# Kernel optimization log

Hardware: AMD Instinct MI355X
Metric: run time of the kernel (lower is better)

The kernel has to match this reference:

```python
import jax, jax.numpy as jnp
import numpy as np

B, S, H, C, T = 8, 1024, 256, 4, 12
THETA = 10000.0


def setup_inputs() -> dict:
    key = jax.random.key(0)
    ks = jax.random.split(key, 7)
    x = jax.random.normal(ks[0], (B, S, H), dtype=jnp.float32)
    token_index = jax.random.randint(ks[1], (B, S), 0, 256, dtype=jnp.int32)
    thread_id = jnp.sort(jax.random.randint(ks[2], (B, S), 0, T, dtype=jnp.int32), axis=-1)
    bound = 1.0 / np.sqrt(H)  # nn.Linear default init range
    Wq = jax.random.uniform(ks[3], (H, H * C), jnp.float32, -bound, bound)
    bq = jax.random.uniform(ks[4], (H * C,), jnp.float32, -bound, bound)
    Wk = jax.random.uniform(ks[5], (H, H * C), jnp.float32, -bound, bound)
    bk = jax.random.uniform(ks[6], (H * C,), jnp.float32, -bound, bound)
    return {"x": x, "Wq": Wq, "bq": bq, "Wk": Wk, "bk": bk,
            "token_index": token_index, "thread_id": thread_id}


def _rope(v, pos):
    # v: (B, S, C, H); pos: (B, S) signed positions
    half = v.shape[-1] // 2
    # freqs = 1 / theta^(arange(0, H, 2) / H)
    freqs = 1.0 / (THETA ** (jnp.arange(half, dtype=jnp.float32) * 2.0 / (2 * half)))
    ang = pos[..., None].astype(jnp.float32) * freqs          # (B, S, half)
    cos = jnp.cos(ang)[:, :, None, :]                          # (B, S, 1, half)
    sin = jnp.sin(ang)[:, :, None, :]
    vr = v.reshape(*v.shape[:-1], half, 2)                     # complex pairs (even, odd)
    re = vr[..., 0] * cos - vr[..., 1] * sin
    im = vr[..., 0] * sin + vr[..., 1] * cos
    return jnp.stack([re, im], axis=-1).reshape(v.shape)


def reference(x, Wq, bq, Wk, bk, token_index, thread_id):
    q = (x @ Wq + bq).reshape(B, S, C, H)
    k = (x @ Wk + bk).reshape(B, S, C, H)
    # Block sign rules of get_instance_embedding reduce to three cases per
    # token pair (m, n) with thread ids ti=thread(m), tj=thread(n):
    #   0 < ti < tj : q uses -pos, k uses +pos
    #   0 < tj < ti : q uses +pos, k uses -pos
    #   otherwise   : both use +pos
    q_pos = _rope(q, token_index)
    q_neg = _rope(q, -token_index)
    k_pos = _rope(k, token_index)
    k_neg = _rope(k, -token_index)
    l1 = jnp.einsum('bmch,bnch->bcmn', q_pos, k_pos)
    l2 = jnp.einsum('bmch,bnch->bcmn', q_neg, k_pos)
    l3 = jnp.einsum('bmch,bnch->bcmn', q_pos, k_neg)
    ti = thread_id[:, :, None]   # rows
    tj = thread_id[:, None, :]   # cols
    cond2 = ((ti > 0) & (ti < tj))[:, None, :, :]   # (B,1,S,S)
    cond3 = ((tj > 0) & (ti > tj))[:, None, :, :]
    return jnp.where(cond2, l2, jnp.where(cond3, l3, l1))  # (B, C, S, S)
```

## Files before the change

### kernel.cpp

```cpp
#include <hip/hip_runtime.h>

#define BB 8
#define SS 1024
#define HH 256
#define CC 4
#define NQ 1024

typedef unsigned short u16;
typedef unsigned int u32;
typedef __attribute__((ext_vector_type(8))) __bf16 bf16x8;
typedef __attribute__((ext_vector_type(4))) float f32x4;
typedef __attribute__((ext_vector_type(4))) u32 u32x4;
typedef __attribute__((ext_vector_type(4))) u16 u16x4;

__device__ __forceinline__ u16 f2bf(float f) {
    u32 u = __float_as_uint(f);
    u32 r = (u + 0x7FFFu + ((u >> 16) & 1u)) >> 16;
    return (u16)r;
}

__device__ __forceinline__ void gld16(const u16* g, u16* l) {
    __builtin_amdgcn_global_load_lds(
        (const __attribute__((address_space(1))) void*)g,
        (__attribute__((address_space(3))) void*)l, 16, 0, 0);
}

__device__ __forceinline__ bf16x8 ldsfrag32(const u16* smem, int row, int c16) {
    const char* p = (const char*)smem + row * 64 + (((c16 ^ ((row >> 1) & 3)) & 3) << 4);
    return *(const bf16x8*)p;
}

#define WAITV(n) asm volatile("s_waitcnt vmcnt(" #n ")" ::: "memory")
#define WAITLG() asm volatile("s_waitcnt lgkmcnt(0)" ::: "memory")

__global__ void __launch_bounds__(256) k0_prep(
    const float4* __restrict__ x4, u16x4* __restrict__ xbf4,
    const float* __restrict__ Wq, const float* __restrict__ Wk,
    u16* __restrict__ Wt, float2* __restrict__ trig) {
    __shared__ u16 tl[64][65];
    int b = blockIdx.x;
    if (b < 2048) {
        int i = b * 256 + threadIdx.x;
        float4 v = x4[i];
        u16x4 o = {f2bf(v.x), f2bf(v.y), f2bf(v.z), f2bf(v.w)};
        xbf4[i] = o;
    } else if (b < 2176) {
        int idx = b - 2048;
        int nb = (idx & 31) * 64, kb = (idx >> 5) * 64;
        int c = threadIdx.x & 63;
#pragma unroll
        for (int r = threadIdx.x >> 6; r < 64; r += 4) {
            int k = kb + r, n = nb + c;
            float v = (n < NQ) ? Wq[k * NQ + n] : Wk[k * NQ + (n - NQ)];
            tl[c][r] = f2bf(v);
        }
        __syncthreads();
#pragma unroll
        for (int r = threadIdx.x >> 6; r < 64; r += 4) {
            Wt[(size_t)(nb + r) * HH + kb + c] = tl[r][c];
        }
    } else {
        int i = (b - 2176) * 256 + threadIdx.x;
        int pos = i >> 7, f = i & 127;
        float freq = __expf(-(float)f * 0.07195578515529633f);
        float ang = (float)pos * freq;
        float s, c;
        sincosf(ang, &s, &c);
        trig[i] = make_float2(c, s);
    }
}

#define STAGE32(dst, srcbase, roff, kc) do {                                    \
        int r_ = (threadIdx.x >> 2);                                            \
        int sl_ = (threadIdx.x & 3) ^ ((r_ >> 1) & 3);                          \
        gld16((srcbase) + (size_t)((roff) + r_) * HH + (kc) * 32 + sl_ * 8,     \
              (dst) + ww * 512);                                                \
    } while (0)

__global__ void __launch_bounds__(512, 2) k1_proj(
    const u16* __restrict__ xbf, const u16* __restrict__ Wt,
    const float* __restrict__ bq, const float* __restrict__ bk,
    const int* __restrict__ tok, const float2* __restrict__ trig,
    u16* __restrict__ qpos, u16* __restrict__ qneg,
    u16* __restrict__ kpos, u16* __restrict__ kneg) {
    int h = blockIdx.x;
    int logical = (h & 7) * 128 + (h >> 3);
    int m0 = (logical >> 4) * 128, n0 = (logical & 15) * 128;
    int ww = threadIdx.x >> 6, l = threadIdx.x & 63;
    int wr = ww >> 1, wc = ww & 1;

    __shared__ u16 sm[24576];
    u16* bA[3] = {sm, sm + 8192, sm + 16384};

    f32x4 acc[2][4] = {};
    STAGE32(bA[0], xbf, m0, 0); STAGE32(bA[0] + 4096, Wt, n0, 0);
    STAGE32(bA[1], xbf, m0, 1); STAGE32(bA[1] + 4096, Wt, n0, 1);
    STAGE32(bA[2], xbf, m0, 2); STAGE32(bA[2] + 4096, Wt, n0, 2);
    WAITV(4);
    __builtin_amdgcn_s_barrier();
#pragma unroll
    for (int kc = 0; kc < 8; ++kc) {
        const u16* As = bA[kc % 3];
        const u16* Bs = As + 4096;
        int c16 = l >> 4;
        bf16x8 af[2], bfr[4];
        __builtin_amdgcn_s_setprio(1);
#pragma unroll
        for (int mi = 0; mi < 2; ++mi) af[mi] = ldsfrag32(As, wr * 32 + mi * 16 + (l & 15), c16);
#pragma unroll
        for (int ns = 0; ns < 4; ++ns) bfr[ns] = ldsfrag32(Bs, wc * 64 + ns * 16 + (l & 15), c16);
#pragma unroll
        for (int mi = 0; mi < 2; ++mi)
#pragma unroll
            for (int ns = 0; ns < 4; ++ns)
                acc[mi][ns] = __builtin_amdgcn_mfma_f32_16x16x32_bf16(af[mi], bfr[ns], acc[mi][ns], 0, 0, 0);
        __builtin_amdgcn_s_setprio(0);
        if (kc < 7) {
            WAITLG();
            __builtin_amdgcn_s_barrier();
            if (kc < 5) {
                STAGE32(bA[kc % 3], xbf, m0, kc + 3);
                STAGE32(bA[kc % 3] + 4096, Wt, n0, kc + 3);
                WAITV(4);
            } else if (kc == 5) {
                WAITV(2);
            } else {
                WAITV(0);
            }
            __builtin_amdgcn_s_barrier();
        }
    }

#pragma unroll
    for (int mi = 0; mi < 2; ++mi)
#pragma unroll
        for (int ns = 0; ns < 4; ++ns) {
            int n = n0 + wc * 64 + ns * 16 + (l & 15);
            bool isq = n < NQ;
            int nc = n & (NQ - 1);
            float bias = isq ? bq[nc] : bk[nc];
            int c = nc >> 8, hh = nc & 255, fi = hh >> 1;
#pragma unroll
            for (int r = 0; r < 4; ++r) {
                int m = m0 + wr * 32 + mi * 16 + (l >> 4) * 4 + r;
                float val = acc[mi][ns][r] + bias;
                float other = __shfl_xor(val, 1);
                int pos = tok[m];
                float2 cs = trig[pos * 128 + fi];
                float rp, rn;
                if ((l & 1) == 0) {
                    rp = val * cs.x - other * cs.y;
                    rn = val * cs.x + other * cs.y;
                } else {
                    rp = other * cs.y + val * cs.x;
                    rn = -other * cs.y + val * cs.x;
                }
                int b = m >> 10, s = m & 1023;
                size_t oidx = ((size_t)((b << 2) | c) * SS + s) * HH + hh;
                if (isq) {
                    qpos[oidx] = f2bf(rp);
                    qneg[oidx] = f2bf(rn);
                } else {
                    kpos[oidx] = f2bf(rp);
                    kneg[oidx] = f2bf(rn);
                }
            }
        }
}

__global__ void __launch_bounds__(512, 2) k2_gemm(
    const u16* __restrict__ qpos, const u16* __restrict__ qneg,
    const u16* __restrict__ kpos, const u16* __restrict__ kneg,
    const int* __restrict__ thread_id, float* __restrict__ out) {
    int h = blockIdx.x;
    int logical = (h & 7) * 256 + (h >> 3);
    int bc = logical >> 6;
    int t = logical & 63;
    int m0 = (t >> 3) * 128, n0 = (t & 7) * 128;
    const int* tb = thread_id + (bc >> 2) * SS;
    int ww = threadIdx.x >> 6, l = threadIdx.x & 63;
    int wr = ww >> 1, wc = ww & 1;
    int ti0 = tb[m0], ti1 = tb[m0 + 127], tj0 = tb[n0], tj1 = tb[n0 + 127];
    bool pure2 = (ti0 > 0) & (ti1 < tj0);
    bool pure3 = (tj0 > 0) & (ti0 > tj1);
    bool pure1 = (ti1 == 0) | (tj1 == 0) | ((ti0 == ti1) & (tj0 == tj1) & (ti0 == tj0));
    size_t base = (size_t)bc * (SS * HH);
    float* ob = out + (size_t)bc * ((size_t)SS * SS);
    int ar0 = m0 + wr * 32;
    int nb0 = n0 + wc * 64;

    __shared__ u16 sm[32768];

    if (pure1 | pure2 | pure3) {
        const u16* q = (pure2 ? qneg : qpos) + base;
        const u16* k = (pure3 ? kneg : kpos) + base;
        u16* bA[3] = {sm, sm + 8192, sm + 16384};

        f32x4 acc[2][4] = {};
        STAGE32(bA[0], q, m0, 0); STAGE32(bA[0] + 4096, k, n0, 0);
        STAGE32(bA[1], q, m0, 1); STAGE32(bA[1] + 4096, k, n0, 1);
        STAGE32(bA[2], q, m0, 2); STAGE32(bA[2] + 4096, k, n0, 2);
        WAITV(4);
        __builtin_amdgcn_s_barrier();
#pragma unroll
        for (int kc = 0; kc < 8; ++kc) {
            const u16* As = bA[kc % 3];
            const u16* Bs = As + 4096;
            int c16 = l >> 4;
            bf16x8 af[2], bfr[4];
            __builtin_amdgcn_s_setprio(1);
#pragma unroll
            for (int mi = 0; mi < 2; ++mi) af[mi] = ldsfrag32(As, wr * 32 + mi * 16 + (l & 15), c16);
#pragma unroll
            for (int ns = 0; ns < 4; ++ns) bfr[ns] = ldsfrag32(Bs, wc * 64 + ns * 16 + (l & 15), c16);
#pragma unroll
            for (int mi = 0; mi < 2; ++mi)
#pragma unroll
                for (int ns = 0; ns < 4; ++ns)
                    acc[mi][ns] = __builtin_amdgcn_mfma_f32_16x16x32_bf16(af[mi], bfr[ns], acc[mi][ns], 0, 0, 0);
            __builtin_amdgcn_s_setprio(0);
            if (kc < 7) {
                WAITLG();
                __builtin_amdgcn_s_barrier();
                if (kc < 5) {
                    STAGE32(bA[kc % 3], q, m0, kc + 3);
                    STAGE32(bA[kc % 3] + 4096, k, n0, kc + 3);
                    WAITV(4);
                } else if (kc == 5) {
                    WAITV(2);
                } else {
                    WAITV(0);
                }
                __builtin_amdgcn_s_barrier();
            }
        }

#pragma unroll
        for (int mi = 0; mi < 2; ++mi)
#pragma unroll
            for (int ns = 0; ns < 4; ++ns)
#pragma unroll
                for (int r = 0; r < 4; ++r) {
                    int m = ar0 + mi * 16 + (l >> 4) * 4 + r;
                    int n = nb0 + ns * 16 + (l & 15);
                    __builtin_nontemporal_store(acc[mi][ns][r], &ob[(size_t)m * SS + n]);
                }
    } else {
        const u16* qp = qpos + base;
        const u16* qn = qneg + base;
        const u16* kp = kpos + base;
        const u16* kn = kneg + base;
        u16* bufb[2] = {sm, sm + 16384};

        int bamin = ti0 > 1 ? ti0 : 1;
        int bcmin = tj0 > 1 ? tj0 : 1;
        bool B2 = (ti1 > 0) && (tj1 > bamin);
        bool B3 = (tj1 > 0) && (ti1 > bcmin);

        int fa[2], fb[2], fc[4], fd[4];
#pragma unroll
        for (int mi = 0; mi < 2; ++mi) {
            fa[mi] = tb[ar0 + mi * 16];
            fb[mi] = tb[ar0 + mi * 16 + 15];
        }
#pragma unroll
        for (int ns = 0; ns < 4; ++ns) {
            fc[ns] = tb[nb0 + ns * 16];
            fd[ns] = tb[nb0 + ns * 16 + 15];
        }
        u32 msk1 = 0, msk2 = 0, msk3 = 0;
#pragma unroll
        for (int mi = 0; mi < 2; ++mi)
#pragma unroll
            for (int ns = 0; ns < 4; ++ns) {
                u32 bit = 1u << (mi * 4 + ns);
                if ((fa[mi] == 0) | (fc[ns] == 0) | ((fa[mi] <= fd[ns]) & (fc[ns] <= fb[mi]))) msk1 |= bit;
                int amin = fa[mi] > 1 ? fa[mi] : 1;
                if ((fb[mi] > 0) & (fd[ns] > amin)) msk2 |= bit;
                int cmin = fc[ns] > 1 ? fc[ns] : 1;
                if ((fd[ns] > 0) & (fb[mi] > cmin)) msk3 |= bit;
            }
        msk1 = __builtin_amdgcn_readfirstlane(msk1);
        msk2 = __builtin_amdgcn_readfirstlane(msk2);
        msk3 = __builtin_amdgcn_readfirstlane(msk3);

#define MSTAGE(bi, kc) do {                                \
        STAGE32(bufb[bi], qp, m0, kc);                     \
        if (B2) STAGE32(bufb[bi] + 4096, qn, m0, kc);      \
        STAGE32(bufb[bi] + 8192, kp, n0, kc);              \
        if (B3) STAGE32(bufb[bi] + 12288, kn, n0, kc);     \
    } while (0)
#define WAITN() do {                                       \
        if (B2 & B3) { WAITV(4); }                         \
        else if (B2 | B3) { WAITV(3); }                    \
        else { WAITV(2); }                                 \
    } while (0)

        f32x4 a1[2][4] = {}, a2[2][4] = {}, a3[2][4] = {};
        MSTAGE(0, 0);
        MSTAGE(1, 1);
        WAITN();
        __builtin_amdgcn_s_barrier();
#pragma unroll
        for (int kc = 0; kc < 8; ++kc) {
            const u16* bqp = bufb[kc & 1];
            const u16* bqn = bqp + 4096;
            const u16* bkp = bqp + 8192;
            const u16* bkn = bqp + 12288;
            int c16 = l >> 4;
            bf16x8 qpF[2], qnF[2], kpF[4], knF[4];
            __builtin_amdgcn_s_setprio(1);
#pragma unroll
            for (int mi = 0; mi < 2; ++mi) {
                int rr = wr * 32 + mi * 16 + (l & 15);
                qpF[mi] = ldsfrag32(bqp, rr, c16);
                if (msk2) qnF[mi] = ldsfrag32(bqn, rr, c16);
            }
#pragma unroll
            for (int ns = 0; ns < 4; ++ns) {
                int rn = wc * 64 + ns * 16 + (l & 15);
                kpF[ns] = ldsfrag32(bkp, rn, c16);
                if (msk3) knF[ns] = ldsfrag32(bkn, rn, c16);
            }
#pragma unroll
            for (int mi = 0; mi < 2; ++mi)
#pragma unroll
                for (int ns = 0; ns < 4; ++ns) {
                    u32 bit = 1u << (mi * 4 + ns);
                    if (msk1 & bit)
                        a1[mi][ns] = __builtin_amdgcn_mfma_f32_16x16x32_bf16(qpF[mi], kpF[ns], a1[mi][ns], 0, 0, 0);
                    if (msk2 & bit)
                        a2[mi][ns] = __builtin_amdgcn_mfma_f32_16x16x32_bf16(qnF[mi], kpF[ns], a2[mi][ns], 0, 0, 0);
                    if (msk3 & bit)
                        a3[mi][ns] = __builtin_amdgcn_mfma_f32_16x16x32_bf16(qpF[mi], knF[ns], a3[mi][ns], 0, 0, 0);
                }
            __builtin_amdgcn_s_setprio(0);
            if (kc < 7) {
                WAITLG();
                __builtin_amdgcn_s_barrier();
                if (kc < 6) {
                    MSTAGE(kc & 1, kc + 2);
                    WAITN();
                } else {
                    WAITV(0);
                }
                __builtin_amdgcn_s_barrier();
            }
        }
#undef MSTAGE
#undef WAITN

        int tj[4], ti_[2][4];
#pragma unroll
        for (int ns = 0; ns < 4; ++ns) tj[ns] = tb[nb0 + ns * 16 + (l & 15)];
#pragma unroll
        for (int mi = 0; mi < 2; ++mi)
#pragma unroll
            for (int r = 0; r < 4; ++r) ti_[mi][r] = tb[ar0 + mi * 16 + (l >> 4) * 4 + r];

#pragma unroll
        for (int mi = 0; mi < 2; ++mi)
#pragma unroll
            for (int ns = 0; ns < 4; ++ns)
#pragma unroll
                for (int r = 0; r < 4; ++r) {
                    int m = ar0 + mi * 16 + (l >> 4) * 4 + r;
                    int n = nb0 + ns * 16 + (l & 15);
                    int ti = ti_[mi][r], tjj = tj[ns];
                    float v = (ti > 0 && ti < tjj) ? a2[mi][ns][r]
                             : ((tjj > 0 && ti > tjj) ? a3[mi][ns][r] : a1[mi][ns][r]);
                    __builtin_nontemporal_store(v, &ob[(size_t)m * SS + n]);
                }
    }
}

extern "C" void kernel_launch(void* const* d_in, const int* in_sizes, int n_in,
                              void* d_out, int out_size, void* d_ws, size_t ws_size,
                              hipStream_t stream) {
    const float* x  = (const float*)d_in[0];
    const float* Wq = (const float*)d_in[1];
    const float* bq = (const float*)d_in[2];
    const float* Wk = (const float*)d_in[3];
    const float* bk = (const float*)d_in[4];
    const int* tok  = (const int*)d_in[5];
    const int* tid  = (const int*)d_in[6];
    float* out = (float*)d_out;

    char* ws = (char*)d_ws;
    const size_t MB = 1u << 20;
    u16* qpos = (u16*)(ws);
    u16* qneg = (u16*)(ws + 16 * MB);
    u16* kpos = (u16*)(ws + 32 * MB);
    u16* kneg = (u16*)(ws + 48 * MB);
    u16* xbf  = (u16*)(ws + 64 * MB);
    u16* Wt   = (u16*)(ws + 68 * MB);
    float2* trig = (float2*)(ws + 69 * MB);

    k0_prep<<<2304, 256, 0, stream>>>((const float4*)x, (u16x4*)xbf, Wq, Wk, Wt, trig);
    k1_proj<<<1024, 512, 0, stream>>>(xbf, Wt, bq, bk, tok, trig, qpos, qneg, kpos, kneg);
    k2_gemm<<<2048, 512, 0, stream>>>(qpos, qneg, kpos, kneg, tid, out);
}
```

Baseline: 111.4 us.

## Split pure/mixed tile paths into separate kernels with 256-thread 4x4-fragment waves

The projection GEMM and the pure-case attention GEMM move to 256-thread blocks where each wave computes a 64x64 tile (4x4 MFMA fragments) instead of 32x64. They also switch from triple to double buffering, which halves LDS use. The pure and mixed tile cases, which used to share one kernel, are now two kernels. The mixed kernel keeps its 512-thread layout and large LDS footprint, so it no longer limits occupancy for the pure tiles. The cost is an extra kernel launch in which blocks exit early, plus higher register pressure per wave.

```diff
diff --git a/kernel.cpp b/kernel.cpp
--- a/kernel.cpp
+++ b/kernel.cpp
@@ -70,6 +70,14 @@
     }
 }
 
+#define KST(dst, srcbase, roff, kc)                                             \
+    _Pragma("unroll") for (int i_ = 0; i_ < 2; ++i_) {                          \
+        int sid_ = i_ * 256 + (int)threadIdx.x;                                 \
+        int r_ = sid_ >> 2;                                                     \
+        int sl_ = (sid_ & 3) ^ ((r_ >> 1) & 3);                                 \
+        gld16((srcbase) + (size_t)((roff) + r_) * HH + (kc) * 32 + sl_ * 8,     \
+              (dst) + i_ * 2048 + ww * 512);                                    \
+    }
 #define STAGE32(dst, srcbase, roff, kc) do {                                    \
         int r_ = (threadIdx.x >> 2);                                            \
         int sl_ = (threadIdx.x & 3) ^ ((r_ >> 1) & 3);                          \
@@ -77,7 +85,7 @@
               (dst) + ww * 512);                                                \
     } while (0)
 
-__global__ void __launch_bounds__(512, 2) k1_proj(
+__global__ void __launch_bounds__(256, 4) k1_proj(
     const u16* __restrict__ xbf, const u16* __restrict__ Wt,
     const float* __restrict__ bq, const float* __restrict__ bk,
     const int* __restrict__ tok, const float2* __restrict__ trig,
@@ -89,28 +97,26 @@
     int ww = threadIdx.x >> 6, l = threadIdx.x & 63;
     int wr = ww >> 1, wc = ww & 1;
 
-    __shared__ u16 sm[24576];
-    u16* bA[3] = {sm, sm + 8192, sm + 16384};
-
-    f32x4 acc[2][4] = {};
-    STAGE32(bA[0], xbf, m0, 0); STAGE32(bA[0] + 4096, Wt, n0, 0);
-    STAGE32(bA[1], xbf, m0, 1); STAGE32(bA[1] + 4096, Wt, n0, 1);
-    STAGE32(bA[2], xbf, m0, 2); STAGE32(bA[2] + 4096, Wt, n0, 2);
+    __shared__ u16 sm[16384];
+
+    f32x4 acc[4][4] = {};
+    KST(sm, xbf, m0, 0)          KST(sm + 4096, Wt, n0, 0)
+    KST(sm + 8192, xbf, m0, 1)   KST(sm + 12288, Wt, n0, 1)
     WAITV(4);
     __builtin_amdgcn_s_barrier();
 #pragma unroll
     for (int kc = 0; kc < 8; ++kc) {
-        const u16* As = bA[kc % 3];
+        const u16* As = sm + (kc & 1) * 8192;
         const u16* Bs = As + 4096;
         int c16 = l >> 4;
-        bf16x8 af[2], bfr[4];
+        bf16x8 af[4], bfr[4];
         __builtin_amdgcn_s_setprio(1);
 #pragma unroll
-        for (int mi = 0; mi < 2; ++mi) af[mi] = ldsfrag32(As, wr * 32 + mi * 16 + (l & 15), c16);
+        for (int mi = 0; mi < 4; ++mi) af[mi] = ldsfrag32(As, wr * 64 + mi * 16 + (l & 15), c16);
 #pragma unroll
         for (int ns = 0; ns < 4; ++ns) bfr[ns] = ldsfrag32(Bs, wc * 64 + ns * 16 + (l & 15), c16);
 #pragma unroll
-        for (int mi = 0; mi < 2; ++mi)
+        for (int mi = 0; mi < 4; ++mi)
 #pragma unroll
             for (int ns = 0; ns < 4; ++ns)
                 acc[mi][ns] = __builtin_amdgcn_mfma_f32_16x16x32_bf16(af[mi], bfr[ns], acc[mi][ns], 0, 0, 0);
@@ -118,12 +124,11 @@
         if (kc < 7) {
             WAITLG();
             __builtin_amdgcn_s_barrier();
-            if (kc < 5) {
-                STAGE32(bA[kc % 3], xbf, m0, kc + 3);
-                STAGE32(bA[kc % 3] + 4096, Wt, n0, kc + 3);
+            if (kc < 6) {
+                u16* db = sm + (kc & 1) * 8192;
+                KST(db, xbf, m0, kc + 2)
+                KST(db + 4096, Wt, n0, kc + 2)
                 WAITV(4);
-            } else if (kc == 5) {
-                WAITV(2);
             } else {
                 WAITV(0);
             }
@@ -132,7 +137,7 @@
     }
 
 #pragma unroll
-    for (int mi = 0; mi < 2; ++mi)
+    for (int mi = 0; mi < 4; ++mi)
 #pragma unroll
         for (int ns = 0; ns < 4; ++ns) {
             int n = n0 + wc * 64 + ns * 16 + (l & 15);
@@ -142,7 +147,7 @@
             int c = nc >> 8, hh = nc & 255, fi = hh >> 1;
 #pragma unroll
             for (int r = 0; r < 4; ++r) {
-                int m = m0 + wr * 32 + mi * 16 + (l >> 4) * 4 + r;
+                int m = m0 + wr * 64 + mi * 16 + (l >> 4) * 4 + r;
                 float val = acc[mi][ns][r] + bias;
                 float other = __shfl_xor(val, 1);
                 int pos = tok[m];
@@ -168,7 +173,7 @@
         }
 }
 
-__global__ void __launch_bounds__(512, 2) k2_gemm(
+__global__ void __launch_bounds__(256, 4) k2_pure(
     const u16* __restrict__ qpos, const u16* __restrict__ qneg,
     const u16* __restrict__ kpos, const u16* __restrict__ kneg,
     const int* __restrict__ thread_id, float* __restrict__ out) {
@@ -178,111 +183,135 @@
     int t = logical & 63;
     int m0 = (t >> 3) * 128, n0 = (t & 7) * 128;
     const int* tb = thread_id + (bc >> 2) * SS;
-    int ww = threadIdx.x >> 6, l = threadIdx.x & 63;
-    int wr = ww >> 1, wc = ww & 1;
     int ti0 = tb[m0], ti1 = tb[m0 + 127], tj0 = tb[n0], tj1 = tb[n0 + 127];
     bool pure2 = (ti0 > 0) & (ti1 < tj0);
     bool pure3 = (tj0 > 0) & (ti0 > tj1);
     bool pure1 = (ti1 == 0) | (tj1 == 0) | ((ti0 == ti1) & (tj0 == tj1) & (ti0 == tj0));
+    if (!(pure1 | pure2 | pure3)) return;
+
+    size_t base = (size_t)bc * (SS * HH);
+    const u16* q = (pure2 ? qneg : qpos) + base;
+    const u16* k = (pure3 ? kneg : kpos) + base;
+    float* ob = out + (size_t)bc * ((size_t)SS * SS);
+
+    int ww = threadIdx.x >> 6, l = threadIdx.x & 63;
+    int wr = ww >> 1, wc = ww & 1;
+    int ar0 = m0 + wr * 64;
+    int nb0 = n0 + wc * 64;
+
+    __shared__ u16 sm[16384];
+
+    f32x4 acc[4][4] = {};
+    KST(sm, q, m0, 0)          KST(sm + 4096, k, n0, 0)
+    KST(sm + 8192, q, m0, 1)   KST(sm + 12288, k, n0, 1)
+    WAITV(4);
+    __builtin_amdgcn_s_barrier();
+#pragma unroll
+    for (int kc = 0; kc < 8; ++kc) {
+        const u16* As = sm + (kc & 1) * 8192;
+        const u16* Bs = As + 4096;
+        int c16 = l >> 4;
+        bf16x8 af[4], bfr[4];
+        __builtin_amdgcn_s_setprio(1);
+#pragma unroll
+        for (int mi = 0; mi < 4; ++mi) af[mi] = ldsfrag32(As, wr * 64 + mi * 16 + (l & 15), c16);
+#pragma unroll
+        for (int ns = 0; ns < 4; ++ns) bfr[ns] = ldsfrag32(Bs, wc * 64 + ns * 16 + (l & 15), c16);
+#pragma unroll
+        for (int mi = 0; mi < 4; ++mi)
+#pragma unroll
+            for (int ns = 0; ns < 4; ++ns)
+                acc[mi][ns] = __builtin_amdgcn_mfma_f32_16x16x32_bf16(af[mi], bfr[ns], acc[mi][ns], 0, 0, 0);
+        __builtin_amdgcn_s_setprio(0);
+        if (kc < 7) {
+            WAITLG();
+            __builtin_amdgcn_s_barrier();
+            if (kc < 6) {
+                u16* db = sm + (kc & 1) * 8192;
+                KST(db, q, m0, kc + 2)
+                KST(db + 4096, k, n0, kc + 2)
+                WAITV(4);
+            } else {
+                WAITV(0);
+            }
+            __builtin_amdgcn_s_barrier();
+        }
+    }
+
+#pragma unroll
+    for (int mi = 0; mi < 4; ++mi)
+#pragma unroll
+        for (int ns = 0; ns < 4; ++ns)
+#pragma unroll
+            for (int r = 0; r < 4; ++r) {
+                int m = ar0 + mi * 16 + (l >> 4) * 4 + r;
+                int n = nb0 + ns * 16 + (l & 15);
+                __builtin_nontemporal_store(acc[mi][ns][r], &ob[(size_t)m * SS + n]);
+            }
+}
+
+__global__ void __launch_bounds__(512, 2) k2_mixed(
+    const u16* __restrict__ qpos, const u16* __restrict__ qneg,
+    const u16* __restrict__ kpos, const u16* __restrict__ kneg,
+    const int* __restrict__ thread_id, float* __restrict__ out) {
+    int h = blockIdx.x;
+    int logical = (h & 7) * 256 + (h >> 3);
+    int bc = logical >> 6;
+    int t = logical & 63;
+    int m0 = (t >> 3) * 128, n0 = (t & 7) * 128;
+    const int* tb = thread_id + (bc >> 2) * SS;
+    int ti0 = tb[m0], ti1 = tb[m0 + 127], tj0 = tb[n0], tj1 = tb[n0 + 127];
+    bool pure2 = (ti0 > 0) & (ti1 < tj0);
+    bool pure3 = (tj0 > 0) & (ti0 > tj1);
+    bool pure1 = (ti1 == 0) | (tj1 == 0) | ((ti0 == ti1) & (tj0 == tj1) & (ti0 == tj0));
+    if (pure1 | pure2 | pure3) return;
+
     size_t base = (size_t)bc * (SS * HH);
     float* ob = out + (size_t)bc * ((size_t)SS * SS);
+    int ww = threadIdx.x >> 6, l = threadIdx.x & 63;
+    int wr = ww >> 1, wc = ww & 1;
     int ar0 = m0 + wr * 32;
     int nb0 = n0 + wc * 64;
 
+    const u16* qp = qpos + base;
+    const u16* qn = qneg + base;
+    const u16* kp = kpos + base;
+    const u16* kn = kneg + base;
+
     __shared__ u16 sm[32768];
-
-    if (pure1 | pure2 | pure3) {
-        const u16* q = (pure2 ? qneg : qpos) + base;
-        const u16* k = (pure3 ? kneg : kpos) + base;
-        u16* bA[3] = {sm, sm + 8192, sm + 16384};
-
-        f32x4 acc[2][4] = {};
-        STAGE32(bA[0], q, m0, 0); STAGE32(bA[0] + 4096, k, n0, 0);
-        STAGE32(bA[1], q, m0, 1); STAGE32(bA[1] + 4096, k, n0, 1);
-        STAGE32(bA[2], q, m0, 2); STAGE32(bA[2] + 4096, k, n0, 2);
-        WAITV(4);
-        __builtin_amdgcn_s_barrier();
-#pragma unroll
-        for (int kc = 0; kc < 8; ++kc) {
-            const u16* As = bA[kc % 3];
-            const u16* Bs = As + 4096;
-            int c16 = l >> 4;
-            bf16x8 af[2], bfr[4];
-            __builtin_amdgcn_s_setprio(1);
-#pragma unroll
-            for (int mi = 0; mi < 2; ++mi) af[mi] = ldsfrag32(As, wr * 32 + mi * 16 + (l & 15), c16);
-#pragma unroll
-            for (int ns = 0; ns < 4; ++ns) bfr[ns] = ldsfrag32(Bs, wc * 64 + ns * 16 + (l & 15), c16);
-#pragma unroll
-            for (int mi = 0; mi < 2; ++mi)
-#pragma unroll
-                for (int ns = 0; ns < 4; ++ns)
-                    acc[mi][ns] = __builtin_amdgcn_mfma_f32_16x16x32_bf16(af[mi], bfr[ns], acc[mi][ns], 0, 0, 0);
-            __builtin_amdgcn_s_setprio(0);
-            if (kc < 7) {
-                WAITLG();
-                __builtin_amdgcn_s_barrier();
-                if (kc < 5) {
-                    STAGE32(bA[kc % 3], q, m0, kc + 3);
-                    STAGE32(bA[kc % 3] + 4096, k, n0, kc + 3);
-                    WAITV(4);
-                } else if (kc == 5) {
-                    WAITV(2);
-                } else {
-                    WAITV(0);
-                }
-                __builtin_amdgcn_s_barrier();
-            }
-        }
-
-#pragma unroll
-        for (int mi = 0; mi < 2; ++mi)
-#pragma unroll
-            for (int ns = 0; ns < 4; ++ns)
-#pragma unroll
-                for (int r = 0; r < 4; ++r) {
-                    int m = ar0 + mi * 16 + (l >> 4) * 4 + r;
-                    int n = nb0 + ns * 16 + (l & 15);
-                    __builtin_nontemporal_store(acc[mi][ns][r], &ob[(size_t)m * SS + n]);
-                }
-    } else {
-        const u16* qp = qpos + base;
-        const u16* qn = qneg + base;
-        const u16* kp = kpos + base;
-        const u16* kn = kneg + base;
-        u16* bufb[2] = {sm, sm + 16384};
-
-        int bamin = ti0 > 1 ? ti0 : 1;
-        int bcmin = tj0 > 1 ? tj0 : 1;
-        bool B2 = (ti1 > 0) && (tj1 > bamin);
-        bool B3 = (tj1 > 0) && (ti1 > bcmin);
-
-        int fa[2], fb[2], fc[4], fd[4];
-#pragma unroll
-        for (int mi = 0; mi < 2; ++mi) {
-            fa[mi] = tb[ar0 + mi * 16];
-            fb[mi] = tb[ar0 + mi * 16 + 15];
-        }
+    u16* bufb[2] = {sm, sm + 16384};
+
+    int bamin = ti0 > 1 ? ti0 : 1;
+    int bcmin = tj0 > 1 ? tj0 : 1;
+    bool B2 = (ti1 > 0) && (tj1 > bamin);
+    bool B3 = (tj1 > 0) && (ti1 > bcmin);
+
+    int fa[2], fb[2], fc[4], fd[4];
+#pragma unroll
+    for (int mi = 0; mi < 2; ++mi) {
+        fa[mi] = tb[ar0 + mi * 16];
+        fb[mi] = tb[ar0 + mi * 16 + 15];
+    }
+#pragma unroll
+    for (int ns = 0; ns < 4; ++ns) {
+        fc[ns] = tb[nb0 + ns * 16];
+        fd[ns] = tb[nb0 + ns * 16 + 15];
+    }
+    u32 msk1 = 0, msk2 = 0, msk3 = 0;
+#pragma unroll
+    for (int mi = 0; mi < 2; ++mi)
 #pragma unroll
         for (int ns = 0; ns < 4; ++ns) {
-            fc[ns] = tb[nb0 + ns * 16];
-            fd[ns] = tb[nb0 + ns * 16 + 15];
-        }
-        u32 msk1 = 0, msk2 = 0, msk3 = 0;
-#pragma unroll
-        for (int mi = 0; mi < 2; ++mi)
-#pragma unroll
-            for (int ns = 0; ns < 4; ++ns) {
-                u32 bit = 1u << (mi * 4 + ns);
-                if ((fa[mi] == 0) | (fc[ns] == 0) | ((fa[mi] <= fd[ns]) & (fc[ns] <= fb[mi]))) msk1 |= bit;
-                int amin = fa[mi] > 1 ? fa[mi] : 1;
-                if ((fb[mi] > 0) & (fd[ns] > amin)) msk2 |= bit;
-                int cmin = fc[ns] > 1 ? fc[ns] : 1;
-                if ((fd[ns] > 0) & (fb[mi] > cmin)) msk3 |= bit;
-            }
-        msk1 = __builtin_amdgcn_readfirstlane(msk1);
-        msk2 = __builtin_amdgcn_readfirstlane(msk2);
-        msk3 = __builtin_amdgcn_readfirstlane(msk3);
+            u32 bit = 1u << (mi * 4 + ns);
+            if ((fa[mi] == 0) | (fc[ns] == 0) | ((fa[mi] <= fd[ns]) & (fc[ns] <= fb[mi]))) msk1 |= bit;
+            int amin = fa[mi] > 1 ? fa[mi] : 1;
+            if ((fb[mi] > 0) & (fd[ns] > amin)) msk2 |= bit;
+            int cmin = fc[ns] > 1 ? fc[ns] : 1;
+            if ((fd[ns] > 0) & (fb[mi] > cmin)) msk3 |= bit;
+        }
+    msk1 = __builtin_amdgcn_readfirstlane(msk1);
+    msk2 = __builtin_amdgcn_readfirstlane(msk2);
+    msk3 = __builtin_amdgcn_readfirstlane(msk3);
 
 #define MSTAGE(bi, kc) do {                                \
         STAGE32(bufb[bi], qp, m0, kc);                     \
@@ -296,82 +325,81 @@
         else { WAITV(2); }                                 \
     } while (0)
 
-        f32x4 a1[2][4] = {}, a2[2][4] = {}, a3[2][4] = {};
-        MSTAGE(0, 0);
-        MSTAGE(1, 1);
-        WAITN();
-        __builtin_amdgcn_s_barrier();
-#pragma unroll
-        for (int kc = 0; kc < 8; ++kc) {
-            const u16* bqp = bufb[kc & 1];
-            const u16* bqn = bqp + 4096;
-            const u16* bkp = bqp + 8192;
-            const u16* bkn = bqp + 12288;
-            int c16 = l >> 4;
-            bf16x8 qpF[2], qnF[2], kpF[4], knF[4];
-            __builtin_amdgcn_s_setprio(1);
-#pragma unroll
-            for (int mi = 0; mi < 2; ++mi) {
-                int rr = wr * 32 + mi * 16 + (l & 15);
-                qpF[mi] = ldsfrag32(bqp, rr, c16);
-                if (msk2) qnF[mi] = ldsfrag32(bqn, rr, c16);
-            }
+    f32x4 a1[2][4] = {}, a2[2][4] = {}, a3[2][4] = {};
+    MSTAGE(0, 0);
+    MSTAGE(1, 1);
+    WAITN();
+    __builtin_amdgcn_s_barrier();
+#pragma unroll
+    for (int kc = 0; kc < 8; ++kc) {
+        const u16* bqp = bufb[kc & 1];
+        const u16* bqn = bqp + 4096;
+        const u16* bkp = bqp + 8192;
+        const u16* bkn = bqp + 12288;
+        int c16 = l >> 4;
+        bf16x8 qpF[2], qnF[2], kpF[4], knF[4];
+        __builtin_amdgcn_s_setprio(1);
+#pragma unroll
+        for (int mi = 0; mi < 2; ++mi) {
+            int rr = wr * 32 + mi * 16 + (l & 15);
+            qpF[mi] = ldsfrag32(bqp, rr, c16);
+            if (msk2) qnF[mi] = ldsfrag32(bqn, rr, c16);
+        }
+#pragma unroll
+        for (int ns = 0; ns < 4; ++ns) {
+            int rn = wc * 64 + ns * 16 + (l & 15);
+            kpF[ns] = ldsfrag32(bkp, rn, c16);
+            if (msk3) knF[ns] = ldsfrag32(bkn, rn, c16);
+        }
+#pragma unroll
+        for (int mi = 0; mi < 2; ++mi)
 #pragma unroll
             for (int ns = 0; ns < 4; ++ns) {
-                int rn = wc * 64 + ns * 16 + (l & 15);
-                kpF[ns] = ldsfrag32(bkp, rn, c16);
-                if (msk3) knF[ns] = ldsfrag32(bkn, rn, c16);
-            }
-#pragma unroll
-            for (int mi = 0; mi < 2; ++mi)
-#pragma unroll
-                for (int ns = 0; ns < 4; ++ns) {
-                    u32 bit = 1u << (mi * 4 + ns);
-                    if (msk1 & bit)
-                        a1[mi][ns] = __builtin_amdgcn_mfma_f32_16x16x32_bf16(qpF[mi], kpF[ns], a1[mi][ns], 0, 0, 0);
-                    if (msk2 & bit)
-                        a2[mi][ns] = __builtin_amdgcn_mfma_f32_16x16x32_bf16(qnF[mi], kpF[ns], a2[mi][ns], 0, 0, 0);
-                    if (msk3 & bit)
-                        a3[mi][ns] = __builtin_amdgcn_mfma_f32_16x16x32_bf16(qpF[mi], knF[ns], a3[mi][ns], 0, 0, 0);
-                }
-            __builtin_amdgcn_s_setprio(0);
-            if (kc < 7) {
-                WAITLG();
-                __builtin_amdgcn_s_barrier();
-                if (kc < 6) {
-                    MSTAGE(kc & 1, kc + 2);
-                    WAITN();
-                } else {
-                    WAITV(0);
-                }
-                __builtin_amdgcn_s_barrier();
-            }
-        }
+                u32 bit = 1u << (mi * 4 + ns);
+                if (msk1 & bit)
+                    a1[mi][ns] = __builtin_amdgcn_mfma_f32_16x16x32_bf16(qpF[mi], kpF[ns], a1[mi][ns], 0, 0, 0);
+                if (msk2 & bit)
+                    a2[mi][ns] = __builtin_amdgcn_mfma_f32_16x16x32_bf16(qnF[mi], kpF[ns], a2[mi][ns], 0, 0, 0);
+                if (msk3 & bit)
+                    a3[mi][ns] = __builtin_amdgcn_mfma_f32_16x16x32_bf16(qpF[mi], knF[ns], a3[mi][ns], 0, 0, 0);
+            }
+        __builtin_amdgcn_s_setprio(0);
+        if (kc < 7) {
+            WAITLG();
+            __builtin_amdgcn_s_barrier();
+            if (kc < 6) {
+                MSTAGE(kc & 1, kc + 2);
+                WAITN();
+            } else {
+                WAITV(0);
+            }
+            __builtin_amdgcn_s_barrier();
+        }
+    }
 #undef MSTAGE
 #undef WAITN
 
-        int tj[4], ti_[2][4];
-#pragma unroll
-        for (int ns = 0; ns < 4; ++ns) tj[ns] = tb[nb0 + ns * 16 + (l & 15)];
-#pragma unroll
-        for (int mi = 0; mi < 2; ++mi)
-#pragma unroll
-            for (int r = 0; r < 4; ++r) ti_[mi][r] = tb[ar0 + mi * 16 + (l >> 4) * 4 + r];
-
-#pragma unroll
-        for (int mi = 0; mi < 2; ++mi)
-#pragma unroll
-            for (int ns = 0; ns < 4; ++ns)
-#pragma unroll
-                for (int r = 0; r < 4; ++r) {
-                    int m = ar0 + mi * 16 + (l >> 4) * 4 + r;
-                    int n = nb0 + ns * 16 + (l & 15);
-                    int ti = ti_[mi][r], tjj = tj[ns];
-                    float v = (ti > 0 && ti < tjj) ? a2[mi][ns][r]
-                             : ((tjj > 0 && ti > tjj) ? a3[mi][ns][r] : a1[mi][ns][r]);
-                    __builtin_nontemporal_store(v, &ob[(size_t)m * SS + n]);
-                }
-    }
+    int tj[4], ti_[2][4];
+#pragma unroll
+    for (int ns = 0; ns < 4; ++ns) tj[ns] = tb[nb0 + ns * 16 + (l & 15)];
+#pragma unroll
+    for (int mi = 0; mi < 2; ++mi)
+#pragma unroll
+        for (int r = 0; r < 4; ++r) ti_[mi][r] = tb[ar0 + mi * 16 + (l >> 4) * 4 + r];
+
+#pragma unroll
+    for (int mi = 0; mi < 2; ++mi)
+#pragma unroll
+        for (int ns = 0; ns < 4; ++ns)
+#pragma unroll
+            for (int r = 0; r < 4; ++r) {
+                int m = ar0 + mi * 16 + (l >> 4) * 4 + r;
+                int n = nb0 + ns * 16 + (l & 15);
+                int ti = ti_[mi][r], tjj = tj[ns];
+                float v = (ti > 0 && ti < tjj) ? a2[mi][ns][r]
+                         : ((tjj > 0 && ti > tjj) ? a3[mi][ns][r] : a1[mi][ns][r]);
+                __builtin_nontemporal_store(v, &ob[(size_t)m * SS + n]);
+            }
 }
 
 extern "C" void kernel_launch(void* const* d_in, const int* in_sizes, int n_in,
@@ -397,6 +425,7 @@
     float2* trig = (float2*)(ws + 69 * MB);
 
     k0_prep<<<2304, 256, 0, stream>>>((const float4*)x, (u16x4*)xbf, Wq, Wk, Wt, trig);
-    k1_proj<<<1024, 512, 0, stream>>>(xbf, Wt, bq, bk, tok, trig, qpos, qneg, kpos, kneg);
-    k2_gemm<<<2048, 512, 0, stream>>>(qpos, qneg, kpos, kneg, tid, out);
-}
+    k1_proj<<<1024, 256, 0, stream>>>(xbf, Wt, bq, bk, tok, trig, qpos, qneg, kpos, kneg);
+    k2_pure<<<2048, 256, 0, stream>>>(qpos, qneg, kpos, kneg, tid, out);
+    k2_mixed<<<2048, 512, 0, stream>>>(qpos, qneg, kpos, kneg, tid, out);
+}
```

Result: slower. 130.6 us (+17.3%).

## Fuse x fp32-to-bf16 conversion into projection GEMM staging

Applied to the files above, without the earlier changes.

The separate prep pass that converted x to bf16 in the workspace is removed. The projection kernel now loads fp32 x rows into registers, converts them to bf16 and writes them into swizzled LDS. The pipeline drops from triple to double buffering to fit this register-staged path. This saves one full write and reread of x and shrinks the prep launch. In exchange each projection block rereads fp32 x (twice the bytes) across 16 column tiles, and the pipeline is shallower.

```diff
diff --git a/kernel.cpp b/kernel.cpp
--- a/kernel.cpp
+++ b/kernel.cpp
@@ -10,6 +10,7 @@
 typedef unsigned int u32;
 typedef __attribute__((ext_vector_type(8))) __bf16 bf16x8;
 typedef __attribute__((ext_vector_type(4))) float f32x4;
+typedef __attribute__((ext_vector_type(8))) float f32x8;
 typedef __attribute__((ext_vector_type(4))) u32 u32x4;
 typedef __attribute__((ext_vector_type(4))) u16 u16x4;
 
@@ -30,23 +31,24 @@
     return *(const bf16x8*)p;
 }
 
+__device__ __forceinline__ void cvt8write(f32x8 v, u16* dst) {
+    u32x4 w;
+#pragma unroll
+    for (int i = 0; i < 4; ++i)
+        w[i] = (u32)f2bf(v[2 * i]) | ((u32)f2bf(v[2 * i + 1]) << 16);
+    *(u32x4*)dst = w;
+}
+
 #define WAITV(n) asm volatile("s_waitcnt vmcnt(" #n ")" ::: "memory")
 #define WAITLG() asm volatile("s_waitcnt lgkmcnt(0)" ::: "memory")
 
 __global__ void __launch_bounds__(256) k0_prep(
-    const float4* __restrict__ x4, u16x4* __restrict__ xbf4,
     const float* __restrict__ Wq, const float* __restrict__ Wk,
     u16* __restrict__ Wt, float2* __restrict__ trig) {
     __shared__ u16 tl[64][65];
     int b = blockIdx.x;
-    if (b < 2048) {
-        int i = b * 256 + threadIdx.x;
-        float4 v = x4[i];
-        u16x4 o = {f2bf(v.x), f2bf(v.y), f2bf(v.z), f2bf(v.w)};
-        xbf4[i] = o;
-    } else if (b < 2176) {
-        int idx = b - 2048;
-        int nb = (idx & 31) * 64, kb = (idx >> 5) * 64;
+    if (b < 128) {
+        int nb = (b & 31) * 64, kb = (b >> 5) * 64;
         int c = threadIdx.x & 63;
 #pragma unroll
         for (int r = threadIdx.x >> 6; r < 64; r += 4) {
@@ -60,7 +62,7 @@
             Wt[(size_t)(nb + r) * HH + kb + c] = tl[r][c];
         }
     } else {
-        int i = (b - 2176) * 256 + threadIdx.x;
+        int i = (b - 128) * 256 + threadIdx.x;
         int pos = i >> 7, f = i & 127;
         float freq = __expf(-(float)f * 0.07195578515529633f);
         float ang = (float)pos * freq;
@@ -78,7 +80,7 @@
     } while (0)
 
 __global__ void __launch_bounds__(512, 2) k1_proj(
-    const u16* __restrict__ xbf, const u16* __restrict__ Wt,
+    const float* __restrict__ x, const u16* __restrict__ Wt,
     const float* __restrict__ bq, const float* __restrict__ bk,
     const int* __restrict__ tok, const float2* __restrict__ trig,
     u16* __restrict__ qpos, u16* __restrict__ qneg,
@@ -89,18 +91,27 @@
     int ww = threadIdx.x >> 6, l = threadIdx.x & 63;
     int wr = ww >> 1, wc = ww & 1;
 
-    __shared__ u16 sm[24576];
-    u16* bA[3] = {sm, sm + 8192, sm + 16384};
+    __shared__ u16 sm[16384];
+
+    int r_ = threadIdx.x >> 2, q_ = threadIdx.x & 3;
+    const float* rowp = x + (size_t)(m0 + r_) * HH + q_ * 8;
+    int aoff = r_ * 32 + ((q_ ^ ((r_ >> 1) & 3)) * 8);
+
+    f32x8 ar[2];
+
+    ar[0] = *(const f32x8*)(rowp);
+    STAGE32(sm + 4096, Wt, n0, 0);
+    WAITV(0);
+    cvt8write(ar[0], sm + aoff);
+    ar[1] = *(const f32x8*)(rowp + 32);
+    STAGE32(sm + 8192 + 4096, Wt, n0, 1);
+    WAITLG();
+    __builtin_amdgcn_s_barrier();
 
     f32x4 acc[2][4] = {};
-    STAGE32(bA[0], xbf, m0, 0); STAGE32(bA[0] + 4096, Wt, n0, 0);
-    STAGE32(bA[1], xbf, m0, 1); STAGE32(bA[1] + 4096, Wt, n0, 1);
-    STAGE32(bA[2], xbf, m0, 2); STAGE32(bA[2] + 4096, Wt, n0, 2);
-    WAITV(4);
-    __builtin_amdgcn_s_barrier();
 #pragma unroll
     for (int kc = 0; kc < 8; ++kc) {
-        const u16* As = bA[kc % 3];
+        const u16* As = sm + (kc & 1) * 8192;
         const u16* Bs = As + 4096;
         int c16 = l >> 4;
         bf16x8 af[2], bfr[4];
@@ -118,15 +129,15 @@
         if (kc < 7) {
             WAITLG();
             __builtin_amdgcn_s_barrier();
-            if (kc < 5) {
-                STAGE32(bA[kc % 3], xbf, m0, kc + 3);
-                STAGE32(bA[kc % 3] + 4096, Wt, n0, kc + 3);
-                WAITV(4);
-            } else if (kc == 5) {
-                WAITV(2);
+            cvt8write(ar[(kc + 1) & 1], sm + ((kc + 1) & 1) * 8192 + aoff);
+            if (kc < 6) {
+                ar[kc & 1] = *(const f32x8*)(rowp + (kc + 2) * 32);
+                STAGE32(sm + (kc & 1) * 8192 + 4096, Wt, n0, kc + 2);
+                WAITV(3);
             } else {
                 WAITV(0);
             }
+            WAITLG();
             __builtin_amdgcn_s_barrier();
         }
     }
@@ -392,11 +403,10 @@
     u16* qneg = (u16*)(ws + 16 * MB);
     u16* kpos = (u16*)(ws + 32 * MB);
     u16* kneg = (u16*)(ws + 48 * MB);
-    u16* xbf  = (u16*)(ws + 64 * MB);
-    u16* Wt   = (u16*)(ws + 68 * MB);
-    float2* trig = (float2*)(ws + 69 * MB);
-
-    k0_prep<<<2304, 256, 0, stream>>>((const float4*)x, (u16x4*)xbf, Wq, Wk, Wt, trig);
-    k1_proj<<<1024, 512, 0, stream>>>(xbf, Wt, bq, bk, tok, trig, qpos, qneg, kpos, kneg);
+    u16* Wt   = (u16*)(ws + 64 * MB);
+    float2* trig = (float2*)(ws + 65 * MB);
+
+    k0_prep<<<256, 256, 0, stream>>>(Wq, Wk, Wt, trig);
+    k1_proj<<<1024, 512, 0, stream>>>(x, Wt, bq, bk, tok, trig, qpos, qneg, kpos, kneg);
     k2_gemm<<<2048, 512, 0, stream>>>(qpos, qneg, kpos, kneg, tid, out);
 }
```

Result: no change. 112.7 us (+1.1%).

## Shrink mixed-tile LDS footprint by splitting three-stream pipeline into two passes

Applied to the files above, without the earlier changes.

Mixed-sign tiles no longer stage all four operand streams (q+, q-, k+, k-) per k-chunk. They run a three-stream pipeline: q+, k+, and whichever of q- or k- is needed. When both negative streams are needed, a second pass handles q+ against k-. This cuts shared memory from 64KB to 48KB per block, which can allow more resident blocks per CU. The cost is reloading q+ and rerunning the k-loop for tiles that need both negative variants.

```diff
diff --git a/kernel.cpp b/kernel.cpp
--- a/kernel.cpp
+++ b/kernel.cpp
@@ -189,7 +189,7 @@
     int ar0 = m0 + wr * 32;
     int nb0 = n0 + wc * 64;
 
-    __shared__ u16 sm[32768];
+    __shared__ u16 sm[24576];
 
     if (pure1 | pure2 | pure3) {
         const u16* q = (pure2 ? qneg : qpos) + base;
@@ -250,7 +250,6 @@
         const u16* qn = qneg + base;
         const u16* kp = kpos + base;
         const u16* kn = kneg + base;
-        u16* bufb[2] = {sm, sm + 16384};
 
         int bamin = ti0 > 1 ? ti0 : 1;
         int bcmin = tj0 > 1 ? tj0 : 1;
@@ -284,71 +283,80 @@
         msk2 = __builtin_amdgcn_readfirstlane(msk2);
         msk3 = __builtin_amdgcn_readfirstlane(msk3);
 
-#define MSTAGE(bi, kc) do {                                \
-        STAGE32(bufb[bi], qp, m0, kc);                     \
-        if (B2) STAGE32(bufb[bi] + 4096, qn, m0, kc);      \
-        STAGE32(bufb[bi] + 8192, kp, n0, kc);              \
-        if (B3) STAGE32(bufb[bi] + 12288, kn, n0, kc);     \
+        f32x4 a1[2][4] = {}, a2[2][4] = {}, a3[2][4] = {};
+
+#define MIXPIPE(S1PTR, S1OFF, HAS1, HASKP, M1, M2, M3)                          \
+    do {                                                                        \
+        STAGE32(sm, qp, m0, 0);                                                 \
+        if (HAS1)  STAGE32(sm + 4096, S1PTR, S1OFF, 0);                         \
+        if (HASKP) STAGE32(sm + 8192, kp, n0, 0);                               \
+        STAGE32(sm + 12288, qp, m0, 1);                                         \
+        if (HAS1)  STAGE32(sm + 16384, S1PTR, S1OFF, 1);                        \
+        if (HASKP) STAGE32(sm + 20480, kp, n0, 1);                              \
+        if ((HAS1) && (HASKP)) { WAITV(3); } else { WAITV(2); }                 \
+        __builtin_amdgcn_s_barrier();                                           \
+        _Pragma("unroll")                                                       \
+        for (int kc = 0; kc < 8; ++kc) {                                        \
+            const u16* bb_ = sm + (kc & 1) * 12288;                             \
+            int c16 = l >> 4;                                                   \
+            bf16x8 qpF[2], xA[2], xB[4], kpF[4];                                \
+            __builtin_amdgcn_s_setprio(1);                                      \
+            _Pragma("unroll")                                                   \
+            for (int mi = 0; mi < 2; ++mi) {                                    \
+                int rr = wr * 32 + mi * 16 + (l & 15);                          \
+                qpF[mi] = ldsfrag32(bb_, rr, c16);                              \
+                if (M2) xA[mi] = ldsfrag32(bb_ + 4096, rr, c16);                \
+            }                                                                   \
+            _Pragma("unroll")                                                   \
+            for (int ns = 0; ns < 4; ++ns) {                                    \
+                int rn = wc * 64 + ns * 16 + (l & 15);                          \
+                if (M3) xB[ns] = ldsfrag32(bb_ + 4096, rn, c16);                \
+                if (HASKP) kpF[ns] = ldsfrag32(bb_ + 8192, rn, c16);            \
+            }                                                                   \
+            _Pragma("unroll")                                                   \
+            for (int mi = 0; mi < 2; ++mi)                                      \
+            _Pragma("unroll")                                                   \
+                for (int ns = 0; ns < 4; ++ns) {                                \
+                    u32 bit = 1u << (mi * 4 + ns);                              \
+                    if ((M1) & bit)                                             \
+                        a1[mi][ns] = __builtin_amdgcn_mfma_f32_16x16x32_bf16(qpF[mi], kpF[ns], a1[mi][ns], 0, 0, 0); \
+                    if ((M2) & bit)                                             \
+                        a2[mi][ns] = __builtin_amdgcn_mfma_f32_16x16x32_bf16(xA[mi], kpF[ns], a2[mi][ns], 0, 0, 0);  \
+                    if ((M3) & bit)                                             \
+                        a3[mi][ns] = __builtin_amdgcn_mfma_f32_16x16x32_bf16(qpF[mi], xB[ns], a3[mi][ns], 0, 0, 0);  \
+                }                                                               \
+            __builtin_amdgcn_s_setprio(0);                                      \
+            if (kc < 7) {                                                       \
+                WAITLG();                                                       \
+                __builtin_amdgcn_s_barrier();                                   \
+                if (kc < 6) {                                                   \
+                    u16* db_ = sm + (kc & 1) * 12288;                           \
+                    STAGE32(db_, qp, m0, kc + 2);                               \
+                    if (HAS1)  STAGE32(db_ + 4096, S1PTR, S1OFF, kc + 2);       \
+                    if (HASKP) STAGE32(db_ + 8192, kp, n0, kc + 2);             \
+                    if ((HAS1) && (HASKP)) { WAITV(3); } else { WAITV(2); }     \
+                } else {                                                        \
+                    WAITV(0);                                                   \
+                }                                                               \
+                __builtin_amdgcn_s_barrier();                                   \
+            }                                                                   \
+        }                                                                       \
     } while (0)
-#define WAITN() do {                                       \
-        if (B2 & B3) { WAITV(4); }                         \
-        else if (B2 | B3) { WAITV(3); }                    \
-        else { WAITV(2); }                                 \
-    } while (0)
-
-        f32x4 a1[2][4] = {}, a2[2][4] = {}, a3[2][4] = {};
-        MSTAGE(0, 0);
-        MSTAGE(1, 1);
-        WAITN();
-        __builtin_amdgcn_s_barrier();
-#pragma unroll
-        for (int kc = 0; kc < 8; ++kc) {
-            const u16* bqp = bufb[kc & 1];
-            const u16* bqn = bqp + 4096;
-            const u16* bkp = bqp + 8192;
-            const u16* bkn = bqp + 12288;
-            int c16 = l >> 4;
-            bf16x8 qpF[2], qnF[2], kpF[4], knF[4];
-            __builtin_amdgcn_s_setprio(1);
-#pragma unroll
-            for (int mi = 0; mi < 2; ++mi) {
-                int rr = wr * 32 + mi * 16 + (l & 15);
-                qpF[mi] = ldsfrag32(bqp, rr, c16);
-                if (msk2) qnF[mi] = ldsfrag32(bqn, rr, c16);
-            }
-#pragma unroll
-            for (int ns = 0; ns < 4; ++ns) {
-                int rn = wc * 64 + ns * 16 + (l & 15);
-                kpF[ns] = ldsfrag32(bkp, rn, c16);
-                if (msk3) knF[ns] = ldsfrag32(bkn, rn, c16);
-            }
-#pragma unroll
-            for (int mi = 0; mi < 2; ++mi)
-#pragma unroll
-                for (int ns = 0; ns < 4; ++ns) {
-                    u32 bit = 1u << (mi * 4 + ns);
-                    if (msk1 & bit)
-                        a1[mi][ns] = __builtin_amdgcn_mfma_f32_16x16x32_bf16(qpF[mi], kpF[ns], a1[mi][ns], 0, 0, 0);
-                    if (msk2 & bit)
-                        a2[mi][ns] = __builtin_amdgcn_mfma_f32_16x16x32_bf16(qnF[mi], kpF[ns], a2[mi][ns], 0, 0, 0);
-                    if (msk3 & bit)
-                        a3[mi][ns] = __builtin_amdgcn_mfma_f32_16x16x32_bf16(qpF[mi], knF[ns], a3[mi][ns], 0, 0, 0);
-                }
-            __builtin_amdgcn_s_setprio(0);
-            if (kc < 7) {
-                WAITLG();
-                __builtin_amdgcn_s_barrier();
-                if (kc < 6) {
-                    MSTAGE(kc & 1, kc + 2);
-                    WAITN();
-                } else {
-                    WAITV(0);
-                }
-                __builtin_amdgcn_s_barrier();
-            }
-        }
-#undef MSTAGE
-#undef WAITN
+
+        {
+            const u16* p1src = B2 ? qn : kn;
+            int p1off = B2 ? m0 : n0;
+            bool has1 = B2 | B3;
+            u32 m2ph = B2 ? msk2 : 0u;
+            u32 m3ph = (!B2 && B3) ? msk3 : 0u;
+            MIXPIPE(p1src, p1off, has1, true, msk1, m2ph, m3ph);
+        }
+        if (B2 & B3) {
+            WAITLG();
+            __builtin_amdgcn_s_barrier();
+            MIXPIPE(kn, n0, true, false, 0u, 0u, msk3);
+        }
+#undef MIXPIPE
 
         int tj[4], ti_[2][4];
 #pragma unroll
```

After: 114.2 us. 2.5% more time.
